# Kernel tuning notes

Measured on AMD Instinct MI355X. Metric: run time of the kernel, lower is better.

The kernel has to match this reference:

```python
import jax, jax.numpy as jnp
import numpy as np

D_MODEL = 1024
N_HEADS = 16
D_HEAD = D_MODEL // N_HEADS
WINDOW = 256
SCALE = D_HEAD ** -0.5


def setup_inputs() -> dict:
    key = jax.random.key(0)
    k1, k2, k3, k4, k5 = jax.random.split(key, 5)
    B, S = 2, 2048
    x = jax.random.normal(k1, (B, S, D_MODEL), dtype=jnp.float32)
    s = 0.02
    Wqkv = jax.random.normal(k2, (D_MODEL, 3 * D_MODEL), dtype=jnp.float32) * s
    bqkv = jnp.zeros((3 * D_MODEL,), dtype=jnp.float32)
    Wout = jax.random.normal(k3, (D_MODEL, D_MODEL), dtype=jnp.float32) * s
    bout = jnp.zeros((D_MODEL,), dtype=jnp.float32)
    return {"x": x, "Wqkv": Wqkv, "bqkv": bqkv, "Wout": Wout, "bout": bout}


def reference(x, Wqkv, bqkv, Wout, bout):
    B, S, D = x.shape
    qkv = x @ Wqkv + bqkv                       # (B, S, 3D)
    q, k, v = jnp.split(qkv, 3, axis=-1)
    # (B, H, S, d)
    q = q.reshape(B, S, N_HEADS, D_HEAD).transpose(0, 2, 1, 3)
    k = k.reshape(B, S, N_HEADS, D_HEAD).transpose(0, 2, 1, 3)
    v = v.reshape(B, S, N_HEADS, D_HEAD).transpose(0, 2, 1, 3)
    scores = jnp.einsum('bhqd,bhkd->bhqk', q, k) * SCALE
    # windowed causal mask: allow j <= i and j >= i - WINDOW (inclusive),
    # matching torch code where mask[i, :i-window_size] = 0 for i >= window_size
    i = jnp.arange(S)[:, None]
    j = jnp.arange(S)[None, :]
    allowed = (j <= i) & (j >= i - WINDOW)      # (S, S)
    scores = jnp.where(allowed[None, None], scores, -jnp.inf)
    attn = jax.nn.softmax(scores, axis=-1)      # dropout=0 / eval mode
    out = jnp.einsum('bhqk,bhkd->bhqd', attn, v)
    out = out.transpose(0, 2, 1, 3).reshape(B, S, D)
    return out @ Wout + bout
```

## Files before the change

kernel.cpp:

```cpp
#include <hip/hip_runtime.h>
#include <stdint.h>


typedef __attribute__((ext_vector_type(8))) short bf16x8;
typedef __attribute__((ext_vector_type(4))) float f32x4;
typedef __attribute__((ext_vector_type(4))) unsigned int u32x4;
typedef __attribute__((ext_vector_type(4))) unsigned short u16x4;

#define DEV static __device__ __forceinline__

#define SC2 0.18033688011112042f

DEV unsigned short f2bf(float f) {
  unsigned int u = __builtin_bit_cast(unsigned int, f);
  u += 0x7fffu + ((u >> 16) & 1u);
  return (unsigned short)(u >> 16);
}

DEV void gload_lds16(const void* g, void* l) {
  __builtin_amdgcn_global_load_lds((const __attribute__((address_space(1))) void*)g,
                                   (__attribute__((address_space(3))) void*)l,
                                   16, 0, 0);
}

__global__ __launch_bounds__(256) void k_prep(const float* __restrict__ x,
                                              const float* __restrict__ Wqkv,
                                              const float* __restrict__ Wout,
                                              const float* __restrict__ bqkv,
                                              unsigned short* __restrict__ xb,
                                              unsigned short* __restrict__ wqT,
                                              unsigned short* __restrict__ woT,
                                              float* __restrict__ bqkv_s) {
  __shared__ float t[32][33];
  const int bid = blockIdx.x, tid = threadIdx.x;
  if (bid < 4096) {
    int i = bid * 256 + tid;
    f32x4 v = ((const f32x4*)x)[i];
    u16x4 o;
    o[0] = f2bf(v[0]); o[1] = f2bf(v[1]); o[2] = f2bf(v[2]); o[3] = f2bf(v[3]);
    ((u16x4*)xb)[i] = o;
    return;
  }
  if (bid >= 8192) {
    int i = (bid - 8192) * 256 + tid;
    if (i < 3072) bqkv_s[i] = bqkv[i] * (i < 1024 ? SC2 : 1.0f);
    return;
  }
  const float* in;
  unsigned short* out;
  int N, K, n0, k0;
  float wscale = 1.0f;
  if (bid < 7168) {
    int tt = bid - 4096;
    in = Wqkv; out = wqT; N = 3072; K = 1024;
    n0 = (tt % 96) * 32; k0 = (tt / 96) * 32;
    if (n0 < 1024) wscale = SC2;
  } else {
    int tt = bid - 7168;
    in = Wout; out = woT; N = 1024; K = 1024;
    n0 = (tt % 32) * 32; k0 = (tt / 32) * 32;
  }
  const int tx = tid & 31, ty = tid >> 5;
#pragma unroll
  for (int i = 0; i < 4; ++i)
    t[ty + i * 8][tx] = in[(size_t)(k0 + ty + i * 8) * N + n0 + tx];
  __syncthreads();
#pragma unroll
  for (int i = 0; i < 4; ++i)
    out[(size_t)(n0 + ty + i * 8) * K + k0 + tx] = f2bf(t[tx][ty + i * 8] * wscale);
}

template <int BN, bool F32OUT, bool FUSE_VT>
__global__ __launch_bounds__(512) void k_gemmbig(const unsigned short* __restrict__ A,
                                                 const unsigned short* __restrict__ Bt,
                                                 const float* __restrict__ bias,
                                                 void* __restrict__ Cout,
                                                 unsigned short* __restrict__ vT,
                                                 int M, int N, int K) {
  constexpr int NI = BN / 32;
  constexpr int ACH = 32;
  constexpr int NCH = ACH + BN / 8;
  constexpr int ASZ = 256 * 64;
  constexpr int BSZ = BN * 64;
  extern __shared__ unsigned short lds[];
  const int tid = threadIdx.x;
  const int lane = tid & 63, wid = tid >> 6;
  const int wr = wid >> 1, wc = wid & 1;
  const int g = lane >> 4, li = lane & 15;
  const int m0 = blockIdx.y * 256, n0 = blockIdx.x * BN;

  f32x4 acc[4][NI] = {};
  const int nkt = K >> 6;
  const int r8 = lane >> 3, sp = lane & 7;

  auto Abuf = [&](int i) { return lds + i * ASZ; };
  auto Bbuf = [&](int i) { return lds + 2 * ASZ + i * BSZ; };

  auto stage = [&](int bufi, int kt) {
#pragma unroll
    for (int c = wid; c < NCH; c += 8) {
      if (c < ACH) {
        int row = c * 8 + r8;
        int sl = sp ^ (row & 7);
        gload_lds16(A + (size_t)(m0 + row) * K + kt * 64 + sl * 8,
                    Abuf(bufi) + c * 512);
      } else {
        int cc = c - ACH;
        int row = cc * 8 + r8;
        int sl = sp ^ (row & 7);
        gload_lds16(Bt + (size_t)(n0 + row) * K + kt * 64 + sl * 8,
                    Bbuf(bufi) + cc * 512);
      }
    }
  };

  stage(0, 0);
  for (int kt = 0; kt < nkt; ++kt) {
    __syncthreads();
    if (kt + 1 < nkt) stage((kt + 1) & 1, kt + 1);
    const unsigned short* Ac = Abuf(kt & 1);
    const unsigned short* Bc = Bbuf(kt & 1);
#pragma unroll
    for (int h = 0; h < 2; ++h) {
      bf16x8 af[4], bfr[NI];
#pragma unroll
      for (int mi = 0; mi < 4; ++mi) {
        const int r = wr * 64 + mi * 16 + li;
        const int slot = (g + h * 4) ^ (r & 7);
        af[mi] = *(const bf16x8*)&Ac[r * 64 + slot * 8];
      }
#pragma unroll
      for (int ni = 0; ni < NI; ++ni) {
        const int r = wc * (BN / 2) + ni * 16 + li;
        const int slot = (g + h * 4) ^ (r & 7);
        bfr[ni] = *(const bf16x8*)&Bc[r * 64 + slot * 8];
      }
#pragma unroll
      for (int mi = 0; mi < 4; ++mi)
#pragma unroll
        for (int ni = 0; ni < NI; ++ni)
          acc[mi][ni] = __builtin_amdgcn_mfma_f32_16x16x32_bf16(af[mi], bfr[ni],
                                                                acc[mi][ni], 0, 0, 0);
    }
  }

  float bv[NI];
#pragma unroll
  for (int ni = 0; ni < NI; ++ni) bv[ni] = bias[n0 + wc * (BN / 2) + ni * 16 + li];
#pragma unroll
  for (int mi = 0; mi < 4; ++mi) {
#pragma unroll
    for (int ni = 0; ni < NI; ++ni) {
      const int col = n0 + wc * (BN / 2) + ni * 16 + li;
      const int row0 = m0 + wr * 64 + mi * 16 + g * 4;
      float v0 = acc[mi][ni][0] + bv[ni];
      float v1 = acc[mi][ni][1] + bv[ni];
      float v2 = acc[mi][ni][2] + bv[ni];
      float v3 = acc[mi][ni][3] + bv[ni];
      if (F32OUT) {
        float* C = (float*)Cout;
        C[(size_t)(row0 + 0) * N + col] = v0;
        C[(size_t)(row0 + 1) * N + col] = v1;
        C[(size_t)(row0 + 2) * N + col] = v2;
        C[(size_t)(row0 + 3) * N + col] = v3;
      } else {
        unsigned short* C = (unsigned short*)Cout;
        C[(size_t)(row0 + 0) * N + col] = f2bf(v0);
        C[(size_t)(row0 + 1) * N + col] = f2bf(v1);
        C[(size_t)(row0 + 2) * N + col] = f2bf(v2);
        C[(size_t)(row0 + 3) * N + col] = f2bf(v3);
      }
      if (FUSE_VT && col >= 2048) {
        const int b = row0 >> 11;
        const int s = row0 & 2047;
        u16x4 vv;
        vv[0] = f2bf(v0); vv[1] = f2bf(v1); vv[2] = f2bf(v2); vv[3] = f2bf(v3);
        *(u16x4*)&vT[(size_t)(b * 1024 + col - 2048) * 2048 + s] = vv;
      }
    }
  }
}

__global__ __launch_bounds__(512) void k_attn5(const unsigned short* __restrict__ qkv,
                                               const unsigned short* __restrict__ vT,
                                               unsigned short* __restrict__ attn) {
  __shared__ unsigned short Ks[2][64 * 64];
  __shared__ unsigned short Vs[2][64 * 64];
  __shared__ unsigned short Ps[128 * 88];
  const int tid = threadIdx.x, lane = tid & 63, wid = tid >> 6;
  const int g = lane >> 4, li = lane & 15;
  const int bh = blockIdx.y, b = bh >> 4, h = bh & 15;
  const int bx = blockIdx.x, q0 = bx * 128;
  const size_t rs = 3072;
  const unsigned short* qb = qkv + (size_t)b * 2048 * rs + h * 64;
  const unsigned short* kb = qb + 1024;
  const unsigned short* vb = vT + (size_t)bh * 64 * 2048;

  const int qrow = wid * 16 + li;
  const bf16x8 qf0 = *(const bf16x8*)(qb + (size_t)(q0 + qrow) * rs + (g << 3));
  const bf16x8 qf1 = *(const bf16x8*)(qb + (size_t)(q0 + qrow) * rs + 32 + (g << 3));

  const int tf_blk = (bx >= 2) ? 0 : (4 - 2 * bx);
  const int tfw = (wid >= 4) ? 1 : 0;
  const int tlw = tfw + 4;

  auto stage = [&](int bufi, int t) {
    const int j0 = q0 - 256 + t * 64;
    const int row = wid * 8 + (lane >> 3);
    const int sl = (lane & 7) ^ (row & 7);
    gload_lds16(kb + (size_t)(j0 + row) * rs + sl * 8, &Ks[bufi][wid * 512]);
    gload_lds16(vb + (size_t)row * 2048 + j0 + sl * 8, &Vs[bufi][wid * 512]);
  };

  f32x4 o[4] = {};
  float l_part[4] = {0.f, 0.f, 0.f, 0.f};

  stage(0, tf_blk);
  int cur = 0;
  for (int t = tf_blk; t < 6; ++t) {
    if (t + 1 < 6) {
      stage(cur ^ 1, t + 1);
      asm volatile("s_waitcnt vmcnt(2)" ::: "memory");
    } else {
      asm volatile("s_waitcnt vmcnt(0)" ::: "memory");
    }
    __builtin_amdgcn_sched_barrier(0);
    __builtin_amdgcn_s_barrier();
    __builtin_amdgcn_sched_barrier(0);

    if (t >= tfw && t <= tlw) {
      const unsigned short* Kc = Ks[cur];
      const unsigned short* Vc = Vs[cur];

      f32x4 s[4];
#pragma unroll
      for (int ni = 0; ni < 4; ++ni) {
        const int kr = ni * 16 + li;
        const int sw = (kr & 7);
        bf16x8 kf0 = *(const bf16x8*)&Kc[kr * 64 + ((g ^ sw) << 3)];
        bf16x8 kf1 = *(const bf16x8*)&Kc[kr * 64 + (((4 + g) ^ sw) << 3)];
        f32x4 z = {};
        z = __builtin_amdgcn_mfma_f32_16x16x32_bf16(qf0, kf0, z, 0, 0, 0);
        z = __builtin_amdgcn_mfma_f32_16x16x32_bf16(qf1, kf1, z, 0, 0, 0);
        s[ni] = z;
      }
      const int rt = (wid & 3) * 16 + g * 4;
#pragma unroll
      for (int ni = 0; ni < 4; ++ni) {
        int ct = ni * 16 + li;
#pragma unroll
        for (int reg = 0; reg < 4; ++reg) {
          float sv = s[ni][reg];
          if (t == tlw && ct > rt + reg) sv = -3e30f;
          if (t == tfw && ct < rt + reg) sv = -3e30f;
          s[ni][reg] = sv;
        }
      }
#pragma unroll
      for (int reg = 0; reg < 4; ++reg) {
        float ps = 0.f;
#pragma unroll
        for (int ni = 0; ni < 4; ++ni) {
          float p = __builtin_exp2f(s[ni][reg] - 16.0f);
          ps += p;
          Ps[(wid * 16 + g * 4 + reg) * 88 + ni * 16 + li] = f2bf(p);
        }
        l_part[reg] += ps;
      }
      asm volatile("s_waitcnt lgkmcnt(0)" ::: "memory");
      __builtin_amdgcn_sched_barrier(0);
      const bf16x8 pf0 = *(const bf16x8*)&Ps[(wid * 16 + li) * 88 + (g << 3)];
      const bf16x8 pf1 = *(const bf16x8*)&Ps[(wid * 16 + li) * 88 + 32 + (g << 3)];
#pragma unroll
      for (int ni = 0; ni < 4; ++ni) {
        const int dr = ni * 16 + li;
        const int sw = (dr & 7);
        bf16x8 vf0 = *(const bf16x8*)&Vc[dr * 64 + ((g ^ sw) << 3)];
        bf16x8 vf1 = *(const bf16x8*)&Vc[dr * 64 + (((4 + g) ^ sw) << 3)];
        o[ni] = __builtin_amdgcn_mfma_f32_16x16x32_bf16(pf0, vf0, o[ni], 0, 0, 0);
        o[ni] = __builtin_amdgcn_mfma_f32_16x16x32_bf16(pf1, vf1, o[ni], 0, 0, 0);
      }
    }
    __builtin_amdgcn_sched_barrier(0);
    __builtin_amdgcn_s_barrier();
    cur ^= 1;
  }

  float inv[4];
#pragma unroll
  for (int reg = 0; reg < 4; ++reg) {
    float L = l_part[reg];
    L += __shfl_xor(L, 1, 64);
    L += __shfl_xor(L, 2, 64);
    L += __shfl_xor(L, 4, 64);
    L += __shfl_xor(L, 8, 64);
    inv[reg] = 1.f / L;
  }
#pragma unroll
  for (int ni = 0; ni < 4; ++ni) {
#pragma unroll
    for (int reg = 0; reg < 4; ++reg) {
      size_t row = (size_t)b * 2048 + q0 + wid * 16 + g * 4 + reg;
      attn[row * 1024 + h * 64 + ni * 16 + li] = f2bf(o[ni][reg] * inv[reg]);
    }
  }
}

extern "C" void kernel_launch(void* const* d_in, const int* in_sizes, int n_in,
                              void* d_out, int out_size, void* d_ws, size_t ws_size,
                              hipStream_t stream) {
  const float* x    = (const float*)d_in[0];
  const float* Wqkv = (const float*)d_in[1];
  const float* bqkv = (const float*)d_in[2];
  const float* Wout = (const float*)d_in[3];
  const float* bout = (const float*)d_in[4];
  float* out = (float*)d_out;

  uint8_t* ws = (uint8_t*)d_ws;
  unsigned short* xb    = (unsigned short*)(ws);
  unsigned short* wqT   = (unsigned short*)(ws +  8388608);
  unsigned short* woT   = (unsigned short*)(ws + 14680064);
  unsigned short* qkvb  = (unsigned short*)(ws + 16777216);
  unsigned short* attnb = (unsigned short*)(ws + 41943040);
  unsigned short* vTb   = (unsigned short*)(ws + 50331648);
  float*          bqs   = (float*)(ws + 58720256);

  hipFuncSetAttribute((const void*)k_gemmbig<192, false, true>,
                      hipFuncAttributeMaxDynamicSharedMemorySize, 114688);
  hipFuncSetAttribute((const void*)k_gemmbig<64, true, false>,
                      hipFuncAttributeMaxDynamicSharedMemorySize, 81920);

  k_prep<<<8204, 256, 0, stream>>>(x, Wqkv, Wout, bqkv, xb, wqT, woT, bqs);
  k_gemmbig<192, false, true><<<dim3(3072 / 192, 4096 / 256), 512, 114688, stream>>>(
      xb, wqT, bqs, qkvb, vTb, 4096, 3072, 1024);
  k_attn5<<<dim3(2048 / 128, 32), 512, 0, stream>>>(qkvb, vTb, attnb);
  k_gemmbig<64, true, false><<<dim3(1024 / 64, 4096 / 256), 512, 81920, stream>>>(
      attnb, woT, bout, out, nullptr, 4096, 1024, 1024);
}
```

Before: 81.21 us.

## Enlarge attention query tile to 256 rows with 1024-thread blocks

The attention kernel now handles 256 query rows per block with 16 waves instead of 128 rows with 8 waves. Shared K/V tiles are then reused across twice as many query rows, and the number of blocks is halved. K and V staging is split across wave groups, with K loaded by the first eight waves and V by the last eight, using dynamic shared memory. The trade-off is fewer blocks (256) for the GPU to schedule, more skipped-work imbalance in the windowed loop, and larger LDS use per block.

```diff
diff --git a/kernel.cpp b/kernel.cpp
--- a/kernel.cpp
+++ b/kernel.cpp
@@ -181,16 +181,14 @@
   }
 }
 
-__global__ __launch_bounds__(512) void k_attn5(const unsigned short* __restrict__ qkv,
-                                               const unsigned short* __restrict__ vT,
-                                               unsigned short* __restrict__ attn) {
-  __shared__ unsigned short Ks[2][64 * 64];
-  __shared__ unsigned short Vs[2][64 * 64];
-  __shared__ unsigned short Ps[128 * 88];
+__global__ __launch_bounds__(1024) void k_attn6(const unsigned short* __restrict__ qkv,
+                                                const unsigned short* __restrict__ vT,
+                                                unsigned short* __restrict__ attn) {
+  extern __shared__ unsigned short alds[];
   const int tid = threadIdx.x, lane = tid & 63, wid = tid >> 6;
   const int g = lane >> 4, li = lane & 15;
   const int bh = blockIdx.y, b = bh >> 4, h = bh & 15;
-  const int bx = blockIdx.x, q0 = bx * 128;
+  const int bx = blockIdx.x, q0 = bx * 256;
   const size_t rs = 3072;
   const unsigned short* qb = qkv + (size_t)b * 2048 * rs + h * 64;
   const unsigned short* kb = qb + 1024;
@@ -200,16 +198,21 @@
   const bf16x8 qf0 = *(const bf16x8*)(qb + (size_t)(q0 + qrow) * rs + (g << 3));
   const bf16x8 qf1 = *(const bf16x8*)(qb + (size_t)(q0 + qrow) * rs + 32 + (g << 3));
 
-  const int tf_blk = (bx >= 2) ? 0 : (4 - 2 * bx);
-  const int tfw = (wid >= 4) ? 1 : 0;
+  const int tf_blk = (bx == 0) ? 4 : 0;
+  const int tfw = wid >> 2;
   const int tlw = tfw + 4;
 
   auto stage = [&](int bufi, int t) {
     const int j0 = q0 - 256 + t * 64;
-    const int row = wid * 8 + (lane >> 3);
+    const int c = wid & 7;
+    const int row = c * 8 + (lane >> 3);
     const int sl = (lane & 7) ^ (row & 7);
-    gload_lds16(kb + (size_t)(j0 + row) * rs + sl * 8, &Ks[bufi][wid * 512]);
-    gload_lds16(vb + (size_t)row * 2048 + j0 + sl * 8, &Vs[bufi][wid * 512]);
+    if (wid < 8)
+      gload_lds16(kb + (size_t)(j0 + row) * rs + sl * 8,
+                  alds + bufi * 4096 + c * 512);
+    else
+      gload_lds16(vb + (size_t)row * 2048 + j0 + sl * 8,
+                  alds + 8192 + bufi * 4096 + c * 512);
   };
 
   f32x4 o[4] = {};
@@ -217,10 +220,10 @@
 
   stage(0, tf_blk);
   int cur = 0;
-  for (int t = tf_blk; t < 6; ++t) {
-    if (t + 1 < 6) {
+  for (int t = tf_blk; t < 8; ++t) {
+    if (t + 1 < 8) {
       stage(cur ^ 1, t + 1);
-      asm volatile("s_waitcnt vmcnt(2)" ::: "memory");
+      asm volatile("s_waitcnt vmcnt(1)" ::: "memory");
     } else {
       asm volatile("s_waitcnt vmcnt(0)" ::: "memory");
     }
@@ -229,8 +232,9 @@
     __builtin_amdgcn_sched_barrier(0);
 
     if (t >= tfw && t <= tlw) {
-      const unsigned short* Kc = Ks[cur];
-      const unsigned short* Vc = Vs[cur];
+      const unsigned short* Kc = alds + cur * 4096;
+      const unsigned short* Vc = alds + 8192 + cur * 4096;
+      unsigned short* Ps = alds + 16384;
 
       f32x4 s[4];
 #pragma unroll
@@ -325,15 +329,17 @@
   unsigned short* vTb   = (unsigned short*)(ws + 50331648);
   float*          bqs   = (float*)(ws + 58720256);
 
-  hipFuncSetAttribute((const void*)k_gemmbig<192, false, true>,
-                      hipFuncAttributeMaxDynamicSharedMemorySize, 114688);
-  hipFuncSetAttribute((const void*)k_gemmbig<64, true, false>,
-                      hipFuncAttributeMaxDynamicSharedMemorySize, 81920);
+  (void)hipFuncSetAttribute((const void*)k_gemmbig<192, false, true>,
+                            hipFuncAttributeMaxDynamicSharedMemorySize, 114688);
+  (void)hipFuncSetAttribute((const void*)k_gemmbig<64, true, false>,
+                            hipFuncAttributeMaxDynamicSharedMemorySize, 81920);
+  (void)hipFuncSetAttribute((const void*)k_attn6,
+                            hipFuncAttributeMaxDynamicSharedMemorySize, 77824);
 
   k_prep<<<8204, 256, 0, stream>>>(x, Wqkv, Wout, bqkv, xb, wqT, woT, bqs);
   k_gemmbig<192, false, true><<<dim3(3072 / 192, 4096 / 256), 512, 114688, stream>>>(
       xb, wqT, bqs, qkvb, vTb, 4096, 3072, 1024);
-  k_attn5<<<dim3(2048 / 128, 32), 512, 0, stream>>>(qkvb, vTb, attnb);
+  k_attn6<<<dim3(2048 / 256, 32), 1024, 77824, stream>>>(qkvb, vTb, attnb);
   k_gemmbig<64, true, false><<<dim3(1024 / 64, 4096 / 256), 512, 81920, stream>>>(
       attnb, woT, bout, out, nullptr, 4096, 1024, 1024);
 }
```

Result: slower. 83.13 us (+2.4%).
